# Kernel tuning notes

Measured on AMD Instinct MI355X. Metric: run time of the kernel, lower is better.

The kernel has to match this reference:

```python
import jax, jax.numpy as jnp
import numpy as np

D_MODEL = 1024
NUM_HEADS = 16
D_K = D_MODEL // NUM_HEADS
THETA = 10000.0


def apply_rope(x, positions):
    # x: [b, h, s, d_k]; positions: [b, s] int32
    half = D_K // 2
    inv_freq = THETA ** (-jnp.arange(half, dtype=jnp.float32) * 2.0 / D_K)  # [half]
    angles = positions[:, None, :, None].astype(jnp.float32) * inv_freq  # [b,1,s,half]
    cos, sin = jnp.cos(angles), jnp.sin(angles)
    x1 = x[..., 0::2]  # even dims
    x2 = x[..., 1::2]  # odd dims
    out_even = x1 * cos - x2 * sin
    out_odd = x1 * sin + x2 * cos
    # re-interleave
    out = jnp.stack([out_even, out_odd], axis=-1)
    return out.reshape(x.shape)


def setup_inputs() -> dict:
    key = jax.random.key(0)
    ks = jax.random.split(key, 5)
    b, s = 2, 2048
    scale = 0.02
    return {
        "x": jax.random.normal(ks[0], (b, s, D_MODEL), dtype=jnp.float32),
        "Wq": jax.random.normal(ks[1], (D_MODEL, D_MODEL), dtype=jnp.float32) * scale,
        "Wk": jax.random.normal(ks[2], (D_MODEL, D_MODEL), dtype=jnp.float32) * scale,
        "Wv": jax.random.normal(ks[3], (D_MODEL, D_MODEL), dtype=jnp.float32) * scale,
        "Wo": jax.random.normal(ks[4], (D_MODEL, D_MODEL), dtype=jnp.float32) * scale,
    }


def reference(x, Wq, Wk, Wv, Wo):
    b, s, _ = x.shape
    # Linear(d, d) applied as x @ W^T (torch Linear convention, no bias)
    Q = x @ Wq.T
    K = x @ Wk.T
    V = x @ Wv.T
    # split heads: [b, s, h*d] -> [b, h, s, d]
    split = lambda t: t.reshape(b, s, NUM_HEADS, D_K).transpose(0, 2, 1, 3)
    Q, K, V = split(Q), split(K), split(V)
    positions = jnp.broadcast_to(jnp.arange(s, dtype=jnp.int32), (b, s))
    Q = apply_rope(Q, positions)
    K = apply_rope(K, positions)
    scores = jnp.einsum('bhqd,bhkd->bhqk', Q, K) / jnp.sqrt(jnp.float32(D_K))
    causal = jnp.tril(jnp.ones((s, s), dtype=bool))
    scores = jnp.where(causal[None, None], scores, -jnp.inf)
    attn = jax.nn.softmax(scores, axis=-1)
    out = jnp.einsum('bhqk,bhkd->bhqd', attn, V)
    out = out.transpose(0, 2, 1, 3).reshape(b, s, D_MODEL)
    return out @ Wo.T
```

## Files before the change

### kernel.cpp

```cpp
#include <hip/hip_runtime.h>

typedef __attribute__((ext_vector_type(8))) short bf16x8;
typedef __attribute__((ext_vector_type(4))) float f32x4;
typedef __attribute__((ext_vector_type(16))) float f32x16;

typedef const __attribute__((address_space(1))) unsigned int gu32;
typedef __attribute__((address_space(3))) unsigned int lu32;

__device__ __forceinline__ void async16(const void* g, void* l) {
  __builtin_amdgcn_global_load_lds((gu32*)g, (lu32*)l, 16, 0, 0);
}

__device__ __forceinline__ unsigned short f2bf(float f) {
  unsigned int u = __float_as_uint(f);
  u += 0x7fffu + ((u >> 16) & 1u);
  return (unsigned short)(u >> 16);
}
__device__ __forceinline__ float b2f(unsigned short s) {
  return __uint_as_float(((unsigned int)s) << 16);
}
__device__ __forceinline__ unsigned int cvtpk(float lo, float hi) {
  unsigned int w;
  asm("v_cvt_pk_bf16_f32 %0, %1, %2" : "=v"(w) : "v"(lo), "v"(hi));
  return w;
}
__device__ __forceinline__ void plswap(unsigned int& x, unsigned int& y) {
  asm("v_permlane32_swap_b32 %0, %1" : "+v"(x), "+v"(y));
}

__global__ __launch_bounds__(256) void cvt_k(const float* __restrict__ in,
                                             unsigned short* __restrict__ out,
                                             int n4) {
  int i = blockIdx.x * 256 + threadIdx.x;
  if (i >= n4) return;
  float4 v = ((const float4*)in)[i];
  ushort4 o;
  o.x = f2bf(v.x); o.y = f2bf(v.y); o.z = f2bf(v.z); o.w = f2bf(v.w);
  ((ushort4*)out)[i] = o;
}

template <int WRITE_F32>
__global__ __launch_bounds__(256) void gemm_bt(const unsigned short* __restrict__ A,
                                               const unsigned short* __restrict__ B,
                                               void* __restrict__ Cp, int N, int K) {
  __shared__ __align__(16) unsigned short Al[2][128 * 32];
  __shared__ __align__(16) unsigned short Bl[2][128 * 32];
  const int t = threadIdx.x;
  const int w = t >> 6, l = t & 63;
  const int wm = w >> 1, wn = w & 1;
  const int lr = l & 15, lg = l >> 4;
  const long bm = (long)blockIdx.x * 128, bn = (long)blockIdx.y * 128;
  const int srow = t >> 2;
  const int c8 = t & 3;
  const int KT = K >> 5;
  f32x4 acc[4][4] = {};

  auto STAGE = [&](int ts) {
    const int bi = ts & 1;
    const int k0 = ts * 32;
    #pragma unroll
    for (int r = 0; r < 2; ++r) {
      int row = r * 64 + srow;
      async16(&A[(bm + row) * (long)K + k0 + c8 * 8], &Al[bi][row * 32 + c8 * 8]);
      async16(&B[(bn + row) * (long)K + k0 + c8 * 8], &Bl[bi][row * 32 + c8 * 8]);
    }
  };

  STAGE(0);
  for (int kt = 0; kt < KT; ++kt) {
    const int cur = kt & 1;
    asm volatile("s_waitcnt vmcnt(0)" ::: "memory");
    __builtin_amdgcn_s_barrier();
    __builtin_amdgcn_sched_barrier(0);
    if (kt + 1 < KT) STAGE(kt + 1);
    bf16x8 af[4], bf[4];
    #pragma unroll
    for (int i = 0; i < 4; ++i) {
      af[i] = *(const bf16x8*)&Al[cur][(wm * 64 + i * 16 + lr) * 32 + lg * 8];
      bf[i] = *(const bf16x8*)&Bl[cur][(wn * 64 + i * 16 + lr) * 32 + lg * 8];
    }
    #pragma unroll
    for (int i = 0; i < 4; ++i)
      #pragma unroll
      for (int j = 0; j < 4; ++j)
        acc[i][j] = __builtin_amdgcn_mfma_f32_16x16x32_bf16(af[i], bf[j], acc[i][j], 0, 0, 0);
  }
  #pragma unroll
  for (int i = 0; i < 4; ++i)
    #pragma unroll
    for (int j = 0; j < 4; ++j)
      #pragma unroll
      for (int r = 0; r < 4; ++r) {
        long row = bm + wm * 64 + i * 16 + lg * 4 + r;
        long col = bn + wn * 64 + j * 16 + lr;
        float v = acc[i][j][r];
        if (WRITE_F32) ((float*)Cp)[row * N + col] = v;
        else ((unsigned short*)Cp)[row * N + col] = f2bf(v);
      }
}

__global__ __launch_bounds__(256) void rope_k(unsigned short* __restrict__ QKV) {
  __shared__ float csl[32], snl[32];
  const int row = blockIdx.x;
  const int s = row & 2047;
  const int t = threadIdx.x;
  if (t < 32) {
    float invf = exp2f((float)t * (-13.287712379549449f / 32.0f));
    float sn, cs;
    sincosf((float)s * invf, &sn, &cs);
    csl[t] = cs; snl[t] = sn;
  }
  __syncthreads();
  const int col0 = (t < 128) ? t * 8 : 1024 + (t - 128) * 8;
  const int i0 = (t & 7) * 4;
  unsigned short* p = &QKV[(size_t)row * 3072 + col0];
  bf16x8 v = *(const bf16x8*)p;
  bf16x8 o;
  #pragma unroll
  for (int j = 0; j < 4; ++j) {
    float x1 = b2f((unsigned short)v[2 * j]);
    float x2 = b2f((unsigned short)v[2 * j + 1]);
    float cs = csl[i0 + j], sn = snl[i0 + j];
    o[2 * j]     = (short)f2bf(x1 * cs - x2 * sn);
    o[2 * j + 1] = (short)f2bf(x1 * sn + x2 * cs);
  }
  *(bf16x8*)p = o;
}

__global__ __launch_bounds__(256) void vtr_k(const unsigned short* __restrict__ QKV,
                                             unsigned short* __restrict__ Vt) {
  __shared__ unsigned short tl[64][66];
  const int kt = blockIdx.x;
  const int bh = blockIdx.y;
  const int b = bh >> 4, h = bh & 15;
  const int t = threadIdx.x;
  const int row = t >> 3, c8 = t & 7;
  #pragma unroll
  for (int r = 0; r < 2; ++r) {
    int k = r * 32 + row;
    bf16x8 v = *(const bf16x8*)&QKV[((long)b * 2048 + kt * 64 + k) * 3072 + 2048 + h * 64 + c8 * 8];
    #pragma unroll
    for (int j = 0; j < 8; ++j) tl[c8 * 8 + j][k] = (unsigned short)v[j];
  }
  __syncthreads();
  #pragma unroll
  for (int r = 0; r < 2; ++r) {
    int d = r * 32 + row;
    ushort4 a, bq;
    a.x = tl[d][c8 * 8 + 0]; a.y = tl[d][c8 * 8 + 1];
    a.z = tl[d][c8 * 8 + 2]; a.w = tl[d][c8 * 8 + 3];
    bq.x = tl[d][c8 * 8 + 4]; bq.y = tl[d][c8 * 8 + 5];
    bq.z = tl[d][c8 * 8 + 6]; bq.w = tl[d][c8 * 8 + 7];
    long off = ((long)bh * 64 + d) * 2048 + kt * 64 + c8 * 8;
    *(ushort4*)&Vt[off] = a;
    *(ushort4*)&Vt[off + 4] = bq;
  }
}

__global__ __launch_bounds__(256) void attn_k(const unsigned short* __restrict__ QKV,
                                              const unsigned short* __restrict__ VtG,
                                              unsigned short* __restrict__ O) {
  __shared__ __align__(16) unsigned short Kl[2][64 * 64];
  __shared__ __align__(16) unsigned short Vl[2][64 * 64];
  const int t = threadIdx.x;
  const int w = t >> 6, l = t & 63;
  const int q31 = l & 31, hi = l >> 5;
  const int bh = blockIdx.x;
  const int qt = 15 - (int)blockIdx.y;
  const int b = bh >> 4, h = bh & 15;
  const int Qb = qt * 128;
  const long rowb = (long)b * 2048;
  const int L = 3072;
  const int NT = 2 * qt + 2;
  const float cexp = 0.125f * 1.4426950408889634f;

  const int qmy = Qb + 32 * w + q31;
  const long qgrow = rowb + qmy;
  const int ktmax = (Qb + 32 * w) >> 6;

  bf16x8 qf[4];
  #pragma unroll
  for (int dk = 0; dk < 4; ++dk)
    qf[dk] = *(const bf16x8*)&QKV[qgrow * L + h * 64 + dk * 16 + hi * 8];

  float m_ = -1e30f, ls = 0.0f;
  f32x16 oa[2];
  #pragma unroll
  for (int dt = 0; dt < 2; ++dt)
    #pragma unroll
    for (int r = 0; r < 16; ++r) oa[dt][r] = 0.0f;

  auto STAGE = [&](int ts) {
    const int bi = ts & 1;
    const long kb = rowb + (long)ts * 64;
    const long vrowb = (long)bh * 64;
    #pragma unroll
    for (int r = 0; r < 2; ++r) {
      int row = w * 16 + r * 8 + (l >> 3);
      int c8s = ((l & 7) ^ (row & 7)) * 8;
      async16(&QKV[(kb + row) * L + 1024 + h * 64 + c8s], &Kl[bi][row * 64 + (l & 7) * 8]);
      async16(&VtG[(vrowb + row) * 2048 + ts * 64 + c8s], &Vl[bi][row * 64 + (l & 7) * 8]);
    }
  };

  STAGE(0);

  for (int kt = 0; kt < NT; ++kt) {
    const int cur = kt & 1;
    asm volatile("s_waitcnt vmcnt(0)" ::: "memory");
    __builtin_amdgcn_s_barrier();
    __builtin_amdgcn_sched_barrier(0);
    if (kt + 1 < NT) STAGE(kt + 1);

    if (kt <= ktmax) {
      f32x16 st[2];
      #pragma unroll
      for (int kt2 = 0; kt2 < 2; ++kt2)
        #pragma unroll
        for (int r = 0; r < 16; ++r) st[kt2][r] = 0.0f;
      __builtin_amdgcn_s_setprio(1);
      #pragma unroll
      for (int dk = 0; dk < 4; ++dk)
        #pragma unroll
        for (int kt2 = 0; kt2 < 2; ++kt2) {
          int krow = kt2 * 32 + q31;
          bf16x8 kfr = *(const bf16x8*)&Kl[cur][krow * 64 + (((2 * dk + hi) ^ (krow & 7)) * 8)];
          st[kt2] = __builtin_amdgcn_mfma_f32_32x32x16_bf16(kfr, qf[dk], st[kt2], 0, 0, 0);
        }
      __builtin_amdgcn_s_setprio(0);
      if (kt == ktmax) {
        #pragma unroll
        for (int kt2 = 0; kt2 < 2; ++kt2)
          #pragma unroll
          for (int r = 0; r < 16; ++r) {
            int kg = kt * 64 + kt2 * 32 + (r & 3) + 8 * (r >> 2) + 4 * hi;
            if (kg > qmy) st[kt2][r] = -1e30f;
          }
      }
      float m0[8];
      #pragma unroll
      for (int i = 0; i < 8; ++i)
        m0[i] = fmaxf(fmaxf(st[0][i], st[0][i + 8]), fmaxf(st[1][i], st[1][i + 8]));
      float mt = fmaxf(fmaxf(fmaxf(m0[0], m0[1]), fmaxf(m0[2], m0[3])),
                       fmaxf(fmaxf(m0[4], m0[5]), fmaxf(m0[6], m0[7])));
      if (__any((mt - m_) * cexp > 8.0f)) {
        float mg = fmaxf(mt, __shfl_xor(mt, 32, 64));
        float mn = fmaxf(m_, mg);
        float al = __builtin_amdgcn_exp2f((m_ - mn) * cexp);
        m_ = mn;
        ls *= al;
        #pragma unroll
        for (int dt = 0; dt < 2; ++dt)
          #pragma unroll
          for (int r = 0; r < 16; ++r) oa[dt][r] *= al;
      }
      const float mc = m_ * cexp;
      #pragma unroll
      for (int kt2 = 0; kt2 < 2; ++kt2)
        #pragma unroll
        for (int r = 0; r < 16; ++r)
          st[kt2][r] = __builtin_amdgcn_exp2f(fmaf(st[kt2][r], cexp, -mc));
      float s0[8];
      #pragma unroll
      for (int i = 0; i < 8; ++i)
        s0[i] = (st[0][i] + st[0][i + 8]) + (st[1][i] + st[1][i + 8]);
      ls += ((s0[0] + s0[1]) + (s0[2] + s0[3])) + ((s0[4] + s0[5]) + (s0[6] + s0[7]));
      bf16x8 pfr[4];
      #pragma unroll
      for (int ks = 0; ks < 4; ++ks) {
        int tt = ks >> 1, gX = 2 * (ks & 1), gY = gX + 1;
        unsigned int x1 = cvtpk(st[tt][4 * gX + 0], st[tt][4 * gX + 1]);
        unsigned int y1 = cvtpk(st[tt][4 * gY + 0], st[tt][4 * gY + 1]);
        plswap(x1, y1);
        unsigned int x2 = cvtpk(st[tt][4 * gX + 2], st[tt][4 * gX + 3]);
        unsigned int y2 = cvtpk(st[tt][4 * gY + 2], st[tt][4 * gY + 3]);
        plswap(x2, y2);
        union { unsigned int u[4]; bf16x8 b; } cc;
        cc.u[0] = x1; cc.u[1] = x2; cc.u[2] = y1; cc.u[3] = y2;
        pfr[ks] = cc.b;
      }
      __builtin_amdgcn_s_setprio(1);
      #pragma unroll
      for (int dt = 0; dt < 2; ++dt)
        #pragma unroll
        for (int ks = 0; ks < 4; ++ks) {
          int vrow = dt * 32 + q31;
          bf16x8 vf = *(const bf16x8*)&Vl[cur][vrow * 64 + (((2 * ks + hi) ^ (vrow & 7)) * 8)];
          oa[dt] = __builtin_amdgcn_mfma_f32_32x32x16_bf16(vf, pfr[ks], oa[dt], 0, 0, 0);
        }
      __builtin_amdgcn_s_setprio(0);
    }
  }
  float lt = ls + __shfl_xor(ls, 32, 64);
  float inv = 1.0f / lt;
  #pragma unroll
  for (int dt = 0; dt < 2; ++dt)
    #pragma unroll
    for (int g = 0; g < 4; ++g) {
      ushort4 o4;
      o4.x = f2bf(oa[dt][4 * g + 0] * inv);
      o4.y = f2bf(oa[dt][4 * g + 1] * inv);
      o4.z = f2bf(oa[dt][4 * g + 2] * inv);
      o4.w = f2bf(oa[dt][4 * g + 3] * inv);
      *(ushort4*)&O[qgrow * 1024 + h * 64 + dt * 32 + 8 * g + 4 * hi] = o4;
    }
}

extern "C" void kernel_launch(void* const* d_in, const int* in_sizes, int n_in,
                              void* d_out, int out_size, void* d_ws, size_t ws_size,
                              hipStream_t stream) {
  const float* x  = (const float*)d_in[0];
  const float* Wq = (const float*)d_in[1];
  const float* Wk = (const float*)d_in[2];
  const float* Wv = (const float*)d_in[3];
  const float* Wo = (const float*)d_in[4];
  char* ws = (char*)d_ws;
  unsigned short* xb   = (unsigned short*)(ws);
  unsigned short* Wb   = (unsigned short*)(ws + (8u << 20));
  unsigned short* Wob  = (unsigned short*)(ws + (14u << 20));
  unsigned short* QKVb = (unsigned short*)(ws + (16u << 20));
  unsigned short* Ob   = (unsigned short*)(ws + (40u << 20));
  unsigned short* Vtg  = xb;

  cvt_k<<<4096, 256, 0, stream>>>(x, xb, 4096 * 1024 / 4);
  cvt_k<<<1024, 256, 0, stream>>>(Wq, Wb, 1024 * 1024 / 4);
  cvt_k<<<1024, 256, 0, stream>>>(Wk, Wb + 1024 * 1024, 1024 * 1024 / 4);
  cvt_k<<<1024, 256, 0, stream>>>(Wv, Wb + 2 * 1024 * 1024, 1024 * 1024 / 4);
  cvt_k<<<1024, 256, 0, stream>>>(Wo, Wob, 1024 * 1024 / 4);

  gemm_bt<0><<<dim3(32, 24), 256, 0, stream>>>(xb, Wb, QKVb, 3072, 1024);
  rope_k<<<4096, 256, 0, stream>>>(QKVb);
  vtr_k<<<dim3(32, 32), 256, 0, stream>>>(QKVb, Vtg);
  attn_k<<<dim3(32, 16), 256, 0, stream>>>(QKVb, Vtg, Ob);
  gemm_bt<1><<<dim3(32, 8), 256, 0, stream>>>(Ob, Wob, d_out, 1024, 1024);
}
```

Baseline: 133.1 us.

## Triple-buffer K/V tiles and software-pipeline QK of next tile with softmax

Moves the K/V shared-memory staging from double to triple buffering, so each tile is prefetched two iterations ahead. It also computes the QK^T MFMA for tile kt+1 before the softmax and PV work of tile kt, alternating between two score register sets. The aim is to overlap matrix-core work with the exp and reduction VALU work and to hide global-load latency. In exchange it adds 16KB of LDS per block and 32 more accumulator VGPRs, which may lower occupancy.

```diff
diff --git a/kernel.cpp b/kernel.cpp
--- a/kernel.cpp
+++ b/kernel.cpp
@@ -160,8 +160,8 @@
 __global__ __launch_bounds__(256) void attn_k(const unsigned short* __restrict__ QKV,
                                               const unsigned short* __restrict__ VtG,
                                               unsigned short* __restrict__ O) {
-  __shared__ __align__(16) unsigned short Kl[2][64 * 64];
-  __shared__ __align__(16) unsigned short Vl[2][64 * 64];
+  __shared__ __align__(16) unsigned short Kl[3][64 * 64];
+  __shared__ __align__(16) unsigned short Vl[3][64 * 64];
   const int t = threadIdx.x;
   const int w = t >> 6, l = t & 63;
   const int q31 = l & 31, hi = l >> 5;
@@ -191,7 +191,7 @@
     for (int r = 0; r < 16; ++r) oa[dt][r] = 0.0f;
 
   auto STAGE = [&](int ts) {
-    const int bi = ts & 1;
+    const int bi = ts % 3;
     const long kb = rowb + (long)ts * 64;
     const long vrowb = (long)bh * 64;
     #pragma unroll
@@ -203,94 +203,112 @@
     }
   };
 
+  auto QK = [&](f32x16 (&st)[2], int bi) {
+    #pragma unroll
+    for (int kt2 = 0; kt2 < 2; ++kt2)
+      #pragma unroll
+      for (int r = 0; r < 16; ++r) st[kt2][r] = 0.0f;
+    __builtin_amdgcn_s_setprio(1);
+    #pragma unroll
+    for (int dk = 0; dk < 4; ++dk)
+      #pragma unroll
+      for (int kt2 = 0; kt2 < 2; ++kt2) {
+        int krow = kt2 * 32 + q31;
+        bf16x8 kfr = *(const bf16x8*)&Kl[bi][krow * 64 + (((2 * dk + hi) ^ (krow & 7)) * 8)];
+        st[kt2] = __builtin_amdgcn_mfma_f32_32x32x16_bf16(kfr, qf[dk], st[kt2], 0, 0, 0);
+      }
+    __builtin_amdgcn_s_setprio(0);
+  };
+
+  auto SMPV = [&](f32x16 (&st)[2], int kt) {
+    if (kt == ktmax) {
+      #pragma unroll
+      for (int kt2 = 0; kt2 < 2; ++kt2)
+        #pragma unroll
+        for (int r = 0; r < 16; ++r) {
+          int kg = kt * 64 + kt2 * 32 + (r & 3) + 8 * (r >> 2) + 4 * hi;
+          if (kg > qmy) st[kt2][r] = -1e30f;
+        }
+    }
+    float m0[8];
+    #pragma unroll
+    for (int i = 0; i < 8; ++i)
+      m0[i] = fmaxf(fmaxf(st[0][i], st[0][i + 8]), fmaxf(st[1][i], st[1][i + 8]));
+    float mt = fmaxf(fmaxf(fmaxf(m0[0], m0[1]), fmaxf(m0[2], m0[3])),
+                     fmaxf(fmaxf(m0[4], m0[5]), fmaxf(m0[6], m0[7])));
+    if (__any((mt - m_) * cexp > 8.0f)) {
+      float mg = fmaxf(mt, __shfl_xor(mt, 32, 64));
+      float mn = fmaxf(m_, mg);
+      float al = __builtin_amdgcn_exp2f((m_ - mn) * cexp);
+      m_ = mn;
+      ls *= al;
+      #pragma unroll
+      for (int dt = 0; dt < 2; ++dt)
+        #pragma unroll
+        for (int r = 0; r < 16; ++r) oa[dt][r] *= al;
+    }
+    const float mc = m_ * cexp;
+    #pragma unroll
+    for (int kt2 = 0; kt2 < 2; ++kt2)
+      #pragma unroll
+      for (int r = 0; r < 16; ++r)
+        st[kt2][r] = __builtin_amdgcn_exp2f(fmaf(st[kt2][r], cexp, -mc));
+    float s0[8];
+    #pragma unroll
+    for (int i = 0; i < 8; ++i)
+      s0[i] = (st[0][i] + st[0][i + 8]) + (st[1][i] + st[1][i + 8]);
+    ls += ((s0[0] + s0[1]) + (s0[2] + s0[3])) + ((s0[4] + s0[5]) + (s0[6] + s0[7]));
+    bf16x8 pfr[4];
+    #pragma unroll
+    for (int ks = 0; ks < 4; ++ks) {
+      int tt = ks >> 1, gX = 2 * (ks & 1), gY = gX + 1;
+      unsigned int x1 = cvtpk(st[tt][4 * gX + 0], st[tt][4 * gX + 1]);
+      unsigned int y1 = cvtpk(st[tt][4 * gY + 0], st[tt][4 * gY + 1]);
+      plswap(x1, y1);
+      unsigned int x2 = cvtpk(st[tt][4 * gX + 2], st[tt][4 * gX + 3]);
+      unsigned int y2 = cvtpk(st[tt][4 * gY + 2], st[tt][4 * gY + 3]);
+      plswap(x2, y2);
+      union { unsigned int u[4]; bf16x8 b; } cc;
+      cc.u[0] = x1; cc.u[1] = x2; cc.u[2] = y1; cc.u[3] = y2;
+      pfr[ks] = cc.b;
+    }
+    const int vb = kt % 3;
+    __builtin_amdgcn_s_setprio(1);
+    #pragma unroll
+    for (int dt = 0; dt < 2; ++dt)
+      #pragma unroll
+      for (int ks = 0; ks < 4; ++ks) {
+        int vrow = dt * 32 + q31;
+        bf16x8 vf = *(const bf16x8*)&Vl[vb][vrow * 64 + (((2 * ks + hi) ^ (vrow & 7)) * 8)];
+        oa[dt] = __builtin_amdgcn_mfma_f32_32x32x16_bf16(vf, pfr[ks], oa[dt], 0, 0, 0);
+      }
+    __builtin_amdgcn_s_setprio(0);
+  };
+
+  f32x16 stA[2], stB[2];
+
   STAGE(0);
-
-  for (int kt = 0; kt < NT; ++kt) {
-    const int cur = kt & 1;
+  STAGE(1);
+  asm volatile("s_waitcnt vmcnt(4)" ::: "memory");
+  __builtin_amdgcn_s_barrier();
+  __builtin_amdgcn_sched_barrier(0);
+  QK(stA, 0);
+
+  auto STEP = [&](f32x16 (&cur)[2], f32x16 (&nxt)[2], int kt) {
     asm volatile("s_waitcnt vmcnt(0)" ::: "memory");
     __builtin_amdgcn_s_barrier();
     __builtin_amdgcn_sched_barrier(0);
-    if (kt + 1 < NT) STAGE(kt + 1);
-
-    if (kt <= ktmax) {
-      f32x16 st[2];
-      #pragma unroll
-      for (int kt2 = 0; kt2 < 2; ++kt2)
-        #pragma unroll
-        for (int r = 0; r < 16; ++r) st[kt2][r] = 0.0f;
-      __builtin_amdgcn_s_setprio(1);
-      #pragma unroll
-      for (int dk = 0; dk < 4; ++dk)
-        #pragma unroll
-        for (int kt2 = 0; kt2 < 2; ++kt2) {
-          int krow = kt2 * 32 + q31;
-          bf16x8 kfr = *(const bf16x8*)&Kl[cur][krow * 64 + (((2 * dk + hi) ^ (krow & 7)) * 8)];
-          st[kt2] = __builtin_amdgcn_mfma_f32_32x32x16_bf16(kfr, qf[dk], st[kt2], 0, 0, 0);
-        }
-      __builtin_amdgcn_s_setprio(0);
-      if (kt == ktmax) {
-        #pragma unroll
-        for (int kt2 = 0; kt2 < 2; ++kt2)
-          #pragma unroll
-          for (int r = 0; r < 16; ++r) {
-            int kg = kt * 64 + kt2 * 32 + (r & 3) + 8 * (r >> 2) + 4 * hi;
-            if (kg > qmy) st[kt2][r] = -1e30f;
-          }
-      }
-      float m0[8];
-      #pragma unroll
-      for (int i = 0; i < 8; ++i)
-        m0[i] = fmaxf(fmaxf(st[0][i], st[0][i + 8]), fmaxf(st[1][i], st[1][i + 8]));
-      float mt = fmaxf(fmaxf(fmaxf(m0[0], m0[1]), fmaxf(m0[2], m0[3])),
-                       fmaxf(fmaxf(m0[4], m0[5]), fmaxf(m0[6], m0[7])));
-      if (__any((mt - m_) * cexp > 8.0f)) {
-        float mg = fmaxf(mt, __shfl_xor(mt, 32, 64));
-        float mn = fmaxf(m_, mg);
-        float al = __builtin_amdgcn_exp2f((m_ - mn) * cexp);
-        m_ = mn;
-        ls *= al;
-        #pragma unroll
-        for (int dt = 0; dt < 2; ++dt)
-          #pragma unroll
-          for (int r = 0; r < 16; ++r) oa[dt][r] *= al;
-      }
-      const float mc = m_ * cexp;
-      #pragma unroll
-      for (int kt2 = 0; kt2 < 2; ++kt2)
-        #pragma unroll
-        for (int r = 0; r < 16; ++r)
-          st[kt2][r] = __builtin_amdgcn_exp2f(fmaf(st[kt2][r], cexp, -mc));
-      float s0[8];
-      #pragma unroll
-      for (int i = 0; i < 8; ++i)
-        s0[i] = (st[0][i] + st[0][i + 8]) + (st[1][i] + st[1][i + 8]);
-      ls += ((s0[0] + s0[1]) + (s0[2] + s0[3])) + ((s0[4] + s0[5]) + (s0[6] + s0[7]));
-      bf16x8 pfr[4];
-      #pragma unroll
-      for (int ks = 0; ks < 4; ++ks) {
-        int tt = ks >> 1, gX = 2 * (ks & 1), gY = gX + 1;
-        unsigned int x1 = cvtpk(st[tt][4 * gX + 0], st[tt][4 * gX + 1]);
-        unsigned int y1 = cvtpk(st[tt][4 * gY + 0], st[tt][4 * gY + 1]);
-        plswap(x1, y1);
-        unsigned int x2 = cvtpk(st[tt][4 * gX + 2], st[tt][4 * gX + 3]);
-        unsigned int y2 = cvtpk(st[tt][4 * gY + 2], st[tt][4 * gY + 3]);
-        plswap(x2, y2);
-        union { unsigned int u[4]; bf16x8 b; } cc;
-        cc.u[0] = x1; cc.u[1] = x2; cc.u[2] = y1; cc.u[3] = y2;
-        pfr[ks] = cc.b;
-      }
-      __builtin_amdgcn_s_setprio(1);
-      #pragma unroll
-      for (int dt = 0; dt < 2; ++dt)
-        #pragma unroll
-        for (int ks = 0; ks < 4; ++ks) {
-          int vrow = dt * 32 + q31;
-          bf16x8 vf = *(const bf16x8*)&Vl[cur][vrow * 64 + (((2 * ks + hi) ^ (vrow & 7)) * 8)];
-          oa[dt] = __builtin_amdgcn_mfma_f32_32x32x16_bf16(vf, pfr[ks], oa[dt], 0, 0, 0);
-        }
-      __builtin_amdgcn_s_setprio(0);
-    }
-  }
+    if (kt + 1 < NT && kt + 1 <= ktmax) QK(nxt, (kt + 1) % 3);
+    if (kt + 2 < NT) STAGE(kt + 2);
+    if (kt <= ktmax) SMPV(cur, kt);
+  };
+
+  int kt = 0;
+  while (kt < NT) {
+    STEP(stA, stB, kt); ++kt;
+    if (kt < NT) { STEP(stB, stA, kt); ++kt; }
+  }
+
   float lt = ls + __shfl_xor(ls, 32, 64);
   float inv = 1.0f / lt;
   #pragma unroll
```

Result: no change. 131.0 us (-1.6%).
